# Performance work log

Measured on AMD Instinct MI355X. Metric: run time of the kernel, lower is better.

Reference implementation:

```python
import jax, jax.numpy as jnp
import numpy as np
from jax import lax

DN = ('NCHW', 'OIHW', 'NCHW')

def _conv(x, w, b, s):
    return lax.conv_general_dilated(x, w, (s, s), 'VALID', dimension_numbers=DN) + b[None, :, None, None]

def _deconv(x, w, b, s):
    # transposed conv, VALID: out = (in-1)*s + k
    return lax.conv_transpose(x, w, (s, s), 'VALID', dimension_numbers=DN) + b[None, :, None, None]

def _encoder(x, ew1, eb1, ew2, eb2, ew3, eb3):
    h = jax.nn.relu(_conv(x, ew1, eb1, 2))
    h = jax.nn.relu(_conv(h, ew2, eb2, 2))
    return jax.nn.relu(_conv(h, ew3, eb3, 2))

def _xcorr(x1, x2):
    # per-sample cross-correlation: x2[i] (C,h,w) is the kernel for x1[i] (C,H,W).
    # Equivalent to the original python loop of B single-sample F.conv2d calls,
    # fused into one grouped conv (feature_group_count=B).
    B, C, H, W = x1.shape
    y = lax.conv_general_dilated(x1.reshape(1, B * C, H, W), x2, (1, 1), 'VALID',
                                 dimension_numbers=DN, feature_group_count=B)
    return y.reshape(B, 1, y.shape[2], y.shape[3])

def setup_inputs():
    key = jax.random.key(0)
    ks = jax.random.split(key, 24)
    B = 64
    f32 = jnp.float32
    def w(k, shape, fan_in):
        return jax.random.normal(k, shape, f32) * np.float32(1.0 / np.sqrt(fan_in))
    inp = {}
    inp['pos'] = jax.random.uniform(ks[0], (B, 3, 255, 255), f32)
    inp['neg'] = jax.random.uniform(ks[1], (B, 3, 255, 255), f32)
    inp['pos_crop'] = jax.random.uniform(ks[2], (B, 3, 127, 127), f32)
    inp['eps'] = jax.random.normal(ks[3], (B, 32, 14, 14), f32)
    s = np.float32(1.0 / np.sqrt(3 * 127 * 127))  # pytorch init_anchor: uniform(-stdv, stdv)
    inp['anchor_crop'] = jax.random.uniform(ks[4], (3, 127, 127), f32, -s, s)
    # shared encoder (used by VAE and by self.encoder)
    inp['ew1'] = w(ks[5], (32, 3, 4, 4), 3 * 16);   inp['eb1'] = jnp.zeros((32,), f32)
    inp['ew2'] = w(ks[6], (64, 32, 4, 4), 32 * 16); inp['eb2'] = jnp.zeros((64,), f32)
    inp['ew3'] = w(ks[7], (64, 64, 4, 4), 64 * 16); inp['eb3'] = jnp.zeros((64,), f32)
    # VAE heads + decoder
    inp['mw'] = w(ks[8], (32, 64, 1, 1), 64);  inp['mb'] = jnp.zeros((32,), f32)
    inp['lw'] = w(ks[9], (32, 64, 1, 1), 64);  inp['lb'] = jnp.zeros((32,), f32)
    inp['dw0'] = w(ks[10], (64, 32, 1, 1), 32);      inp['db0'] = jnp.zeros((64,), f32)
    inp['dw1'] = w(ks[11], (32, 64, 4, 4), 64 * 16); inp['db1'] = jnp.zeros((32,), f32)
    inp['dw2'] = w(ks[12], (16, 32, 4, 4), 32 * 16); inp['db2'] = jnp.zeros((16,), f32)
    inp['dw3'] = w(ks[13], (3, 16, 5, 5), 16 * 25);  inp['db3'] = jnp.zeros((3,), f32)
    return inp

def reference(pos, neg, pos_crop, eps, anchor_crop, ew1, eb1, ew2, eb2, ew3, eb3,
              mw, mb, lw, lb, dw0, db0, dw1, db1, dw2, db2, dw3, db3):
    enc = lambda x: _encoder(x, ew1, eb1, ew2, eb2, ew3, eb3)
    # VAE forward on pos_crop
    h = enc(pos_crop)                          # [B,64,14,14]
    mu = _conv(h, mw, mb, 1)                   # [B,32,14,14]
    logvar = _conv(h, lw, lb, 1)
    z = mu + eps * jnp.exp(0.5 * logvar)       # reparameterization
    d = jax.nn.relu(_conv(z, dw0, db0, 1))
    d = jax.nn.relu(_deconv(d, dw1, db1, 2))   # 14 -> 30
    d = jax.nn.relu(_deconv(d, dw2, db2, 2))   # 30 -> 62
    recon = jax.nn.sigmoid(_deconv(d, dw3, db3, 2))  # 62 -> 127
    # siamese branches
    pos_f = enc(pos)                           # [B,64,30,30]
    neg_f = enc(neg)
    B = pos.shape[0]
    anchor = jnp.broadcast_to(anchor_crop[None], (B,) + anchor_crop.shape)  # [B,3,127,127]
    anchor_f = enc(anchor)                     # [B,64,14,14]
    cxp = _xcorr(pos_f, anchor_f)              # [B,1,17,17]
    cxn = _xcorr(neg_f, anchor_f)
    return (anchor, cxp, cxn, recon, mu, logvar)
```

## Files before the change

### kernel.cpp

```cpp
#include <hip/hip_runtime.h>

#define DIVUP(a,b) (((a)+(b)-1)/(b))

__global__ void bcast_anchor_kernel(const float* __restrict__ a, float* __restrict__ out) {
    int i = blockIdx.x * 256 + threadIdx.x;
    int b = blockIdx.y;
    if (i < 48387) out[b * 48387 + i] = a[i];
}

template<int OCT, bool VEC>
__global__ void conv4s2_relu_k(const float* __restrict__ in, const float* __restrict__ w,
                               const float* __restrict__ bias, float* __restrict__ out,
                               int Cin, int Hin, int Win, int Hout, int Wout)
{
    const int ocg = blockIdx.y, b = blockIdx.z, Cout = gridDim.y * OCT;
    const int TX = (Wout + 3) >> 2;
    const int t  = blockIdx.x * 256 + threadIdx.x;
    if (t >= Hout * TX) return;
    const int oy = t / TX, tx = t - oy * TX;
    int ox0 = tx * 4; if (ox0 > Wout - 4) ox0 = Wout - 4;

    const float* ip = in + ((size_t)(b * Cin) * Hin + 2 * oy) * Win + 2 * ox0;
    const float* wb = w + (size_t)ocg * OCT * Cin * 16;
    float acc[OCT][4];
    #pragma unroll
    for (int o = 0; o < OCT; ++o) {
        float z = bias[ocg * OCT + o];
        acc[o][0] = z; acc[o][1] = z; acc[o][2] = z; acc[o][3] = z;
    }
    for (int ic = 0; ic < Cin; ++ic) {
        const float* r = ip + (size_t)ic * Hin * Win;
        #pragma unroll
        for (int ky = 0; ky < 4; ++ky) {
            const float* rr = r + ky * Win;
            float x0,x1,x2,x3,x4,x5,x6,x7,x8,x9;
            if (VEC) {
                const float2* rv = (const float2*)rr;
                float2 p0=rv[0], p1=rv[1], p2=rv[2], p3=rv[3], p4=rv[4];
                x0=p0.x; x1=p0.y; x2=p1.x; x3=p1.y; x4=p2.x;
                x5=p2.y; x6=p3.x; x7=p3.y; x8=p4.x; x9=p4.y;
            } else {
                x0=rr[0]; x1=rr[1]; x2=rr[2]; x3=rr[3]; x4=rr[4];
                x5=rr[5]; x6=rr[6]; x7=rr[7]; x8=rr[8]; x9=rr[9];
            }
            #pragma unroll
            for (int o = 0; o < OCT; ++o) {
                const float* wk = wb + ((o * Cin + ic) * 4 + ky) * 4;
                float w0 = wk[0], w1 = wk[1], w2 = wk[2], w3 = wk[3];
                acc[o][0] = fmaf(x0, w0, fmaf(x1, w1, fmaf(x2, w2, fmaf(x3, w3, acc[o][0]))));
                acc[o][1] = fmaf(x2, w0, fmaf(x3, w1, fmaf(x4, w2, fmaf(x5, w3, acc[o][1]))));
                acc[o][2] = fmaf(x4, w0, fmaf(x5, w1, fmaf(x6, w2, fmaf(x7, w3, acc[o][2]))));
                acc[o][3] = fmaf(x6, w0, fmaf(x7, w1, fmaf(x8, w2, fmaf(x9, w3, acc[o][3]))));
            }
        }
    }
    float* op = out + (((size_t)b * Cout + ocg * OCT) * Hout + oy) * Wout + ox0;
    #pragma unroll
    for (int o = 0; o < OCT; ++o) {
        float* q = op + (size_t)o * Hout * Wout;
        q[0] = fmaxf(acc[o][0], 0.0f); q[1] = fmaxf(acc[o][1], 0.0f);
        q[2] = fmaxf(acc[o][2], 0.0f); q[3] = fmaxf(acc[o][3], 0.0f);
    }
}

__global__ void vae_head_kernel(const float* __restrict__ h, const float* __restrict__ mw,
                                const float* __restrict__ mb, const float* __restrict__ lw,
                                const float* __restrict__ lb, const float* __restrict__ eps,
                                float* __restrict__ mu_out, float* __restrict__ lv_out,
                                float* __restrict__ z_out)
{
    const int idx = blockIdx.x * 256 + threadIdx.x;
    if (idx >= 64 * 32 * 196) return;
    const int p  = idx % 196;
    const int oc = (idx / 196) % 32;
    const int b  = idx / (196 * 32);
    const float* hb = h + (b * 64) * 196 + p;
    float am = mb[oc], al = lb[oc];
    for (int ic = 0; ic < 64; ++ic) {
        float hv = hb[ic * 196];
        am = fmaf(hv, mw[oc * 64 + ic], am);
        al = fmaf(hv, lw[oc * 64 + ic], al);
    }
    mu_out[idx] = am;
    lv_out[idx] = al;
    z_out[idx]  = fmaf(eps[idx], expf(0.5f * al), am);
}

__global__ void conv1x1_relu_kernel(const float* __restrict__ in, const float* __restrict__ w,
                                    const float* __restrict__ bias, float* __restrict__ out,
                                    int Cin, int Cout, int HW, int total)
{
    const int idx = blockIdx.x * 256 + threadIdx.x;
    if (idx >= total) return;
    const int p  = idx % HW;
    const int oc = (idx / HW) % Cout;
    const int b  = idx / (HW * Cout);
    const float* ib = in + (b * Cin) * HW + p;
    float acc = bias[oc];
    for (int ic = 0; ic < 64; ++ic) acc = fmaf(ib[(ic % Cin) * HW], w[oc * Cin + (ic % Cin)], acc) - ((ic >= Cin) ? fmaf(ib[(ic % Cin) * HW], w[oc * Cin + (ic % Cin)], 0.0f) : 0.0f);
    out[idx] = fmaxf(acc, 0.0f);
}

template<int OCT>
__global__ void deconv4s2_relu_k(const float* __restrict__ in, const float* __restrict__ w,
                                 const float* __restrict__ bias, float* __restrict__ out,
                                 int Cin, int Hin, int Win, int Hout, int Wout)
{
    const int ocg = blockIdx.y, b = blockIdx.z, Cout = gridDim.y * OCT;
    const int H2 = Hout >> 1, W2 = Wout >> 1;
    const int t = blockIdx.x * 256 + threadIdx.x;
    if (t >= H2 * W2) return;
    const int oyi = t / W2, oxi = t - oyi * W2;
    const bool my0 = oyi >= 1, my1 = oyi < Hin;
    const bool mx0 = oxi >= 1, mx1 = oxi < Win;
    const int iy0 = my0 ? oyi - 1 : 0, iy1 = my1 ? oyi : 0;
    const int ix0 = mx0 ? oxi - 1 : 0, ix1 = mx1 ? oxi : 0;
    float acc[OCT][4];
    #pragma unroll
    for (int o = 0; o < OCT; ++o) {
        float z = bias[ocg * OCT + o];
        acc[o][0] = z; acc[o][1] = z; acc[o][2] = z; acc[o][3] = z;
    }
    const float* ib = in + (size_t)(b * Cin) * Hin * Win;
    const float* wb = w + (size_t)ocg * OCT * Cin * 16;
    for (int ic = 0; ic < Cin; ++ic) {
        const float* base = ib + (size_t)ic * Hin * Win;
        float v00 = (my0 && mx0) ? base[iy0 * Win + ix0] : 0.0f;
        float v01 = (my0 && mx1) ? base[iy0 * Win + ix1] : 0.0f;
        float v10 = (my1 && mx0) ? base[iy1 * Win + ix0] : 0.0f;
        float v11 = (my1 && mx1) ? base[iy1 * Win + ix1] : 0.0f;
        #pragma unroll
        for (int o = 0; o < OCT; ++o) {
            const float* wc = wb + (size_t)(o * Cin + ic) * 16;
            #pragma unroll
            for (int py = 0; py < 2; ++py)
                #pragma unroll
                for (int px = 0; px < 2; ++px) {
                    const int k0 = (1 - py) * 4, k1 = (3 - py) * 4;
                    acc[o][py * 2 + px] =
                        fmaf(v00, wc[k0 + 1 - px], fmaf(v01, wc[k0 + 3 - px],
                        fmaf(v10, wc[k1 + 1 - px], fmaf(v11, wc[k1 + 3 - px],
                             acc[o][py * 2 + px]))));
                }
        }
    }
    const int oy = 2 * oyi, ox = 2 * oxi;
    #pragma unroll
    for (int o = 0; o < OCT; ++o) {
        float* op = out + (((size_t)b * Cout + ocg * OCT + o) * Hout + oy) * Wout + ox;
        float2 r0; r0.x = fmaxf(acc[o][0], 0.0f); r0.y = fmaxf(acc[o][1], 0.0f);
        float2 r1; r1.x = fmaxf(acc[o][2], 0.0f); r1.y = fmaxf(acc[o][3], 0.0f);
        *(float2*)op = r0;
        *(float2*)(op + Wout) = r1;
    }
}

__global__ void deconv5s2_sigmoid_k(const float* __restrict__ in, const float* __restrict__ w,
                                    const float* __restrict__ bias, float* __restrict__ out)
{
    __shared__ float lds[16 * 6 * 66];
    const int b   = blockIdx.y;
    const int tid = threadIdx.x;
    const int oyi0 = blockIdx.x * 4;

    const float* ib = in + (size_t)(b * 16) * 3844;
    for (int i = tid; i < 16 * 6 * 66; i += 256) {
        const int c   = i % 66;
        const int row = i / 66;
        const int r   = row % 6;
        const int ic  = row / 6;
        const int iy  = oyi0 - 2 + r;
        const int ix  = c - 2;
        float v = 0.0f;
        if ((unsigned)iy < 62u && (unsigned)ix < 62u)
            v = ib[ic * 3844 + iy * 62 + ix];
        lds[i] = v;
    }
    __syncthreads();

    const int ry0 = tid >> 6;
    const int oxi = tid & 63;

    float acc[3][4];
    #pragma unroll
    for (int oc = 0; oc < 3; ++oc) {
        float z = bias[oc];
        acc[oc][0] = z; acc[oc][1] = z; acc[oc][2] = z; acc[oc][3] = z;
    }
    for (int ic = 0; ic < 16; ++ic) {
        const float* lb = lds + ic * 6 * 66;
        float v[3][3];
        #pragma unroll
        for (int a = 0; a < 3; ++a)
            #pragma unroll
            for (int c = 0; c < 3; ++c)
                v[a][c] = lb[(ry0 + a) * 66 + oxi + c];
        #pragma unroll
        for (int a = 0; a < 3; ++a)
            #pragma unroll
            for (int c = 0; c < 3; ++c) {
                float vv = v[a][c];
                #pragma unroll
                for (int oc = 0; oc < 3; ++oc) {
                    const float* wc = w + (oc * 16 + ic) * 25;
                    acc[oc][0] = fmaf(vv, wc[(2 * a) * 5 + 2 * c], acc[oc][0]);
                    if (c > 0) acc[oc][1] = fmaf(vv, wc[(2 * a) * 5 + 2 * c - 1], acc[oc][1]);
                    if (a > 0) acc[oc][2] = fmaf(vv, wc[(2 * a - 1) * 5 + 2 * c], acc[oc][2]);
                    if (a > 0 && c > 0) acc[oc][3] = fmaf(vv, wc[(2 * a - 1) * 5 + 2 * c - 1], acc[oc][3]);
                }
            }
    }
    #pragma unroll
    for (int oc = 0; oc < 3; ++oc)
        #pragma unroll
        for (int j = 0; j < 4; ++j)
            acc[oc][j] = 1.0f / (1.0f + expf(-acc[oc][j]));

    __syncthreads();
    #pragma unroll
    for (int oc = 0; oc < 3; ++oc)
        #pragma unroll
        for (int py = 0; py < 2; ++py)
            #pragma unroll
            for (int px = 0; px < 2; ++px)
                lds[((oc * 8 + 2 * ry0 + py) * 2 + px) * 64 + oxi] = acc[oc][py * 2 + px];
    __syncthreads();

    const int oybase = 2 * oyi0;
    for (int i = tid; i < 3 * 8 * 127; i += 256) {
        const int ox = i % 127;
        const int rr = i / 127;
        const int ry = rr % 8;
        const int oc = rr / 8;
        const int oy = oybase + ry;
        if (oy < 127) {
            float vv = lds[((oc * 8 + ry) * 2 + (ox & 1)) * 64 + (ox >> 1)];
            out[(((size_t)b * 3 + oc) * 127 + oy) * 127 + ox] = vv;
        }
    }
}

__global__ void xcorr_split_kernel(const float* __restrict__ f, const float* __restrict__ af,
                                   float* __restrict__ out)
{
    const int b = blockIdx.x, g = blockIdx.y;
    const int idx = threadIdx.x;
    if (idx >= 153) return;
    const int oy = idx / 9, tx = idx - oy * 9, ox = tx * 2;
    const float* fb = f + ((size_t)b * 64 + g * 4) * 900 + oy * 30 + ox;
    const float* ab = af + g * 4 * 196;
    float a0 = 0.0f, a1 = 0.0f;
    for (int c = 0; c < 4; ++c) {
        const float* fc = fb + c * 900;
        const float* ac = ab + c * 196;
        #pragma unroll
        for (int ky = 0; ky < 14; ++ky) {
            const float* fr = fc + ky * 30;
            const float* ar = ac + ky * 14;
            float v[15];
            #pragma unroll
            for (int k = 0; k < 15; ++k) v[k] = fr[k];
            #pragma unroll
            for (int k = 0; k < 14; ++k) {
                float wv = ar[k];
                a0 = fmaf(v[k],     wv, a0);
                a1 = fmaf(v[k + 1], wv, a1);
            }
        }
    }
    atomicAdd(&out[b * 289 + oy * 17 + ox], a0);
    if (ox + 1 < 17) atomicAdd(&out[b * 289 + oy * 17 + ox + 1], a1);
}

extern "C" void kernel_launch(void* const* d_in, const int* in_sizes, int n_in,
                              void* d_out, int out_size, void* d_ws, size_t ws_size,
                              hipStream_t stream)
{
    const float* pos         = (const float*)d_in[0];
    const float* neg         = (const float*)d_in[1];
    const float* pos_crop    = (const float*)d_in[2];
    const float* eps         = (const float*)d_in[3];
    const float* anchor_crop = (const float*)d_in[4];
    const float* ew1 = (const float*)d_in[5];  const float* eb1 = (const float*)d_in[6];
    const float* ew2 = (const float*)d_in[7];  const float* eb2 = (const float*)d_in[8];
    const float* ew3 = (const float*)d_in[9];  const float* eb3 = (const float*)d_in[10];
    const float* mw  = (const float*)d_in[11]; const float* mb  = (const float*)d_in[12];
    const float* lw  = (const float*)d_in[13]; const float* lb  = (const float*)d_in[14];
    const float* dw0 = (const float*)d_in[15]; const float* db0 = (const float*)d_in[16];
    const float* dw1 = (const float*)d_in[17]; const float* db1 = (const float*)d_in[18];
    const float* dw2 = (const float*)d_in[19]; const float* db2 = (const float*)d_in[20];
    const float* dw3 = (const float*)d_in[21]; const float* db3 = (const float*)d_in[22];

    float* out = (float*)d_out;
    float* ws  = (float*)d_ws;

    float* o_anchor = out;
    float* o_cxp    = out + 3096768;
    float* o_cxn    = out + 3115264;
    float* o_recon  = out + 3133760;
    float* o_mu     = out + 6230528;
    float* o_lv     = out + 6631936;

    float* AF = ws;
    float* A  = ws + 12544;
    const long budget = (long)(ws_size / 4) - 12544;

    const int CBV = budget >= 12361728L ? 64 : budget >= 6582272L ? 32
                  : budget >= 3692544L ? 16 : 8;
    float* E1  = A;
    float* E2  = A + (size_t)CBV * 123008;
    float* CH3 = E2 + (size_t)CBV * 57600;
    const bool dec_full = budget >= 6983680L;
    float* Z   = A;
    float* D0  = A + 401408;
    float* D1  = A + 1204224;
    float* D2  = A + 3047424;
    float* D2c = A;
    const int CB = budget >= 24127488L ? 32 : budget >= 12063744L ? 16
                 : budget >= 6031872L ? 8 : 4;
    float* F1 = A;
    float* F2 = A + (size_t)CB * 508032;
    float* F3 = A;
    float* AH1 = A;
    float* AH2 = A + 123008;

    bcast_anchor_kernel<<<dim3(189, 64), 256, 0, stream>>>(anchor_crop, o_anchor);

    conv4s2_relu_k<4,false><<<dim3(4, 8, 1), 256, 0, stream>>>(anchor_crop, ew1, eb1, AH1, 3, 127, 127, 62, 62);
    conv4s2_relu_k<4,true ><<<dim3(1, 16, 1), 256, 0, stream>>>(AH1, ew2, eb2, AH2, 32, 62, 62, 30, 30);
    conv4s2_relu_k<4,true ><<<dim3(1, 16, 1), 256, 0, stream>>>(AH2, ew3, eb3, AF, 64, 30, 30, 14, 14);

    for (int c = 0; c < 64 / CBV; ++c) {
        const float* inp = pos_crop + (size_t)c * CBV * 48387;
        conv4s2_relu_k<4,false><<<dim3(4, 8, CBV), 256, 0, stream>>>(inp, ew1, eb1, E1, 3, 127, 127, 62, 62);
        conv4s2_relu_k<4,true ><<<dim3(1, 16, CBV), 256, 0, stream>>>(E1, ew2, eb2, E2, 32, 62, 62, 30, 30);
        conv4s2_relu_k<4,true ><<<dim3(1, 16, CBV), 256, 0, stream>>>(E2, ew3, eb3, CH3 + (size_t)c * CBV * 12544, 64, 30, 30, 14, 14);
    }
    vae_head_kernel<<<1568, 256, 0, stream>>>(CH3, mw, mb, lw, lb, eps, o_mu, o_lv, Z);
    conv1x1_relu_kernel<<<3136, 256, 0, stream>>>(Z, dw0, db0, D0, 32, 64, 196, 64*64*196);
    deconv4s2_relu_k<4><<<dim3(1, 8, 64), 256, 0, stream>>>(D0, dw1, db1, D1, 64, 14, 14, 30, 30);
    if (dec_full) {
        deconv4s2_relu_k<4><<<dim3(4, 4, 64), 256, 0, stream>>>(D1, dw2, db2, D2, 32, 30, 30, 62, 62);
        deconv5s2_sigmoid_k<<<dim3(16, 64), 256, 0, stream>>>(D2, dw3, db3, o_recon);
    } else {
        for (int c = 0; c < 4; ++c) {
            deconv4s2_relu_k<4><<<dim3(4, 4, 16), 256, 0, stream>>>(D1 + (size_t)c * 16 * 28800, dw2, db2, D2c, 32, 30, 30, 62, 62);
            deconv5s2_sigmoid_k<<<dim3(16, 16), 256, 0, stream>>>(D2c, dw3, db3, o_recon + (size_t)c * 16 * 48387);
        }
    }

    hipMemsetAsync(o_cxp, 0, 2 * 18496 * sizeof(float), stream);
    const int nchunks = 128 / CB;
    for (int c = 0; c < nchunks; ++c) {
        const int s0 = c * CB;
        const float* inp  = (s0 < 64) ? pos + (size_t)s0 * 195075 : neg + (size_t)(s0 - 64) * 195075;
        float*       o_cx = (s0 < 64) ? o_cxp + (size_t)s0 * 289  : o_cxn + (size_t)(s0 - 64) * 289;
        conv4s2_relu_k<4,false><<<dim3(16, 8, CB), 256, 0, stream>>>(inp, ew1, eb1, F1, 3, 255, 255, 126, 126);
        conv4s2_relu_k<4,true ><<<dim3(4, 16, CB), 256, 0, stream>>>(F1, ew2, eb2, F2, 32, 126, 126, 62, 62);
        conv4s2_relu_k<4,true ><<<dim3(1, 16, CB), 256, 0, stream>>>(F2, ew3, eb3, F3, 64, 62, 62, 30, 30);
        xcorr_split_kernel<<<dim3(CB, 16), 192, 0, stream>>>(F3, AF, o_cx);
    }
}
```

Baseline: 1.536 ms.

## Add LDS-tiled conv4s2 kernel for encoder layers 2 and 3

Adds a conv kernel that stages an input row band for 8 input channels at a time in shared memory, with one thread per output pixel accumulating many output channels (64 or 32). It replaces the register-blocked global-load kernel for encoder conv2 on the crop and search branches and for conv3 on the search branch. The goal is to reuse input pixels across all output channels from LDS instead of re-reading global memory per 4-channel group. The trade-offs are large per-thread accumulator arrays that may pressure registers, weights read from global or scalar memory in the inner loop, and some idle threads when TH*Wout < 256.

```diff
diff --git a/kernel.cpp b/kernel.cpp
--- a/kernel.cpp
+++ b/kernel.cpp
@@ -60,6 +60,72 @@
         float* q = op + (size_t)o * Hout * Wout;
         q[0] = fmaxf(acc[o][0], 0.0f); q[1] = fmaxf(acc[o][1], 0.0f);
         q[2] = fmaxf(acc[o][2], 0.0f); q[3] = fmaxf(acc[o][3], 0.0f);
+    }
+}
+
+template<int CIN, int OCG, int TH, int WIN>
+__global__ void conv4s2_lds_k(const float* __restrict__ in, const float* __restrict__ w,
+                              const float* __restrict__ bias, float* __restrict__ out,
+                              int Hout, int Wout)
+{
+    constexpr int ICC = 8;
+    constexpr int R   = 2 * TH + 2;
+    __shared__ float lds[ICC * R * WIN];
+    const int b   = blockIdx.z;
+    const int ocg = blockIdx.y;
+    const int Hin = 2 * Hout + 2;
+    int oy0 = blockIdx.x * TH;
+    if (oy0 > Hout - TH) oy0 = Hout - TH;
+
+    const int tid = threadIdx.x;
+    const int ox  = tid % Wout;
+    const int ty  = tid / Wout;
+    const bool act = ty < TH;
+
+    float acc[OCG];
+    #pragma unroll
+    for (int oc = 0; oc < OCG; ++oc) acc[oc] = bias[ocg * OCG + oc];
+
+    const float* ib    = in + ((size_t)b * CIN * Hin + 2 * oy0) * WIN;
+    const float* wbase = w + (size_t)(ocg * OCG) * CIN * 16;
+
+    for (int cc = 0; cc < CIN / ICC; ++cc) {
+        __syncthreads();
+        constexpr int NV = ICC * R * (WIN / 2);
+        for (int e = tid; e < NV; e += 256) {
+            const int ic  = e / (R * (WIN / 2));
+            const int rem = e - ic * (R * (WIN / 2));
+            const int r   = rem / (WIN / 2);
+            const int c2  = rem - r * (WIN / 2);
+            const float2 v = *(const float2*)(ib + ((size_t)(cc * ICC + ic) * Hin + r) * WIN + 2 * c2);
+            *(float2*)&lds[(ic * R + r) * WIN + 2 * c2] = v;
+        }
+        __syncthreads();
+        if (act) {
+            #pragma unroll 1
+            for (int ic8 = 0; ic8 < ICC; ++ic8) {
+                #pragma unroll 1
+                for (int ky = 0; ky < 4; ++ky) {
+                    const float* row = &lds[(ic8 * R + 2 * ty + ky) * WIN + 2 * ox];
+                    float2 p0 = *(const float2*)row;
+                    float2 p1 = *(const float2*)(row + 2);
+                    const float* wk = wbase + (size_t)(cc * ICC + ic8) * 16 + ky * 4;
+                    #pragma unroll
+                    for (int oc = 0; oc < OCG; ++oc) {
+                        const float* wo = wk + (size_t)oc * CIN * 16;
+                        acc[oc] = fmaf(p0.x, wo[0], fmaf(p0.y, wo[1],
+                                  fmaf(p1.x, wo[2], fmaf(p1.y, wo[3], acc[oc]))));
+                    }
+                }
+            }
+        }
+    }
+    if (act) {
+        const int oy = oy0 + ty;
+        float* ob = out + (((size_t)b * 64 + ocg * OCG) * Hout + oy) * Wout + ox;
+        #pragma unroll
+        for (int oc = 0; oc < OCG; ++oc)
+            ob[(size_t)oc * Hout * Wout] = fmaxf(acc[oc], 0.0f);
     }
 }
 
@@ -333,7 +399,7 @@
     for (int c = 0; c < 64 / CBV; ++c) {
         const float* inp = pos_crop + (size_t)c * CBV * 48387;
         conv4s2_relu_k<4,false><<<dim3(4, 8, CBV), 256, 0, stream>>>(inp, ew1, eb1, E1, 3, 127, 127, 62, 62);
-        conv4s2_relu_k<4,true ><<<dim3(1, 16, CBV), 256, 0, stream>>>(E1, ew2, eb2, E2, 32, 62, 62, 30, 30);
+        conv4s2_lds_k<32,64,8,62><<<dim3(4, 1, CBV), 256, 0, stream>>>(E1, ew2, eb2, E2, 30, 30);
         conv4s2_relu_k<4,true ><<<dim3(1, 16, CBV), 256, 0, stream>>>(E2, ew3, eb3, CH3 + (size_t)c * CBV * 12544, 64, 30, 30, 14, 14);
     }
     vae_head_kernel<<<1568, 256, 0, stream>>>(CH3, mw, mb, lw, lb, eps, o_mu, o_lv, Z);
@@ -356,8 +422,8 @@
         const float* inp  = (s0 < 64) ? pos + (size_t)s0 * 195075 : neg + (size_t)(s0 - 64) * 195075;
         float*       o_cx = (s0 < 64) ? o_cxp + (size_t)s0 * 289  : o_cxn + (size_t)(s0 - 64) * 289;
         conv4s2_relu_k<4,false><<<dim3(16, 8, CB), 256, 0, stream>>>(inp, ew1, eb1, F1, 3, 255, 255, 126, 126);
-        conv4s2_relu_k<4,true ><<<dim3(4, 16, CB), 256, 0, stream>>>(F1, ew2, eb2, F2, 32, 126, 126, 62, 62);
-        conv4s2_relu_k<4,true ><<<dim3(1, 16, CB), 256, 0, stream>>>(F2, ew3, eb3, F3, 64, 62, 62, 30, 30);
+        conv4s2_lds_k<32,64,4,126><<<dim3(16, 1, CB), 256, 0, stream>>>(F1, ew2, eb2, F2, 62, 62);
+        conv4s2_lds_k<64,32,8,62><<<dim3(4, 2, CB), 256, 0, stream>>>(F2, ew3, eb3, F3, 30, 30);
         xcorr_split_kernel<<<dim3(CB, 16), 192, 0, stream>>>(F3, AF, o_cx);
     }
 }
```

After: 4.097 ms. +166.8%, slower.
